# Kernel optimization log

Hardware: AMD Instinct MI355X
Metric: run time of the kernel (lower is better)

The kernel has to match this reference:

```python
import jax, jax.numpy as jnp
import numpy as np


def _fixed_bernoulli(key, heads, rows, cols, connectivity):
    # Each column gets exactly k = max(1, int(connectivity*rows)) ones (as in _fixed_bernoulli).
    k = max(1, int(connectivity * rows))
    r = jax.random.uniform(key, (heads, rows, cols))
    thr = jnp.sort(r, axis=1)[:, k - 1:k, :]  # k-th smallest per (head, col)
    return (r <= thr).astype(jnp.float32)


def _spectral_radius(W, iters=80):
    # Power-iteration estimate of |lambda_max| per head (replaces torch.linalg.eigvals at init).
    U, N, _ = W.shape
    v0 = jnp.ones((U, N), jnp.float32) / np.sqrt(N)

    def body(v, _):
        w = jnp.einsum('unm,um->un', W, v)
        nrm = jnp.linalg.norm(w, axis=-1, keepdims=True)
        return w / nrm, nrm[:, 0]

    _, nrms = jax.lax.scan(body, v0, None, length=iters)
    return jnp.mean(nrms[-10:], axis=0)  # damp oscillation from complex eigenpairs


def setup_inputs() -> dict:
    key = jax.random.key(0)
    ks = jax.random.split(key, 10)
    B, U, N, D, O = 64, 16, 2048, 1024, 1024
    X = jax.random.normal(ks[0], (B, U, D), jnp.float32)
    state = jax.random.normal(ks[1], (B, U, N), jnp.float32)
    Wmask = _fixed_bernoulli(ks[2], U, N, N, 0.2)
    W = jax.random.normal(ks[3], (U, N, N), jnp.float32) * Wmask
    W = W / _spectral_radius(W)[:, None, None]  # W buffer is normalized to spectral radius ~1
    Win = _fixed_bernoulli(ks[4], U, D, N, 0.2)  # 0/1 fixed-bernoulli input weights
    bias = (jax.random.uniform(ks[5], (U, 1, N)) < 0.5).astype(jnp.float32)
    Wout = jax.random.normal(ks[6], (U, N, O), jnp.float32)
    adaptive_lr = jax.random.uniform(ks[7], (U, D, 1), jnp.float32)
    sr = jax.random.uniform(ks[8], (U, 1, 1), jnp.float32)
    temperature = jnp.ones((1,), jnp.float32)
    return {"X": X, "state": state, "W": W, "Win": Win, "bias": bias,
            "Wout": Wout, "adaptive_lr": adaptive_lr, "sr": sr, "temperature": temperature}


def reference(X, state, W, Win, bias, Wout, adaptive_lr, sr, temperature):
    # X: [B,U,D], state: [B,U,N]
    # lr: softmax over the units axis of (X @ adaptive_lr) / temperature -> [B,U,1]
    lr = jax.nn.softmax(jnp.einsum('bud,udk->buk', X, adaptive_lr) / temperature, axis=1)
    feed = jnp.einsum('bud,udn->bun', X, Win)
    # _sparse_mm_subhead(state, W*sr, ...) + bias == per-unit state @ (W*sr) + bias
    echo = jnp.einsum('bun,unm->bum', state, W * sr) + bias[:, 0, :]
    new_state = (1.0 - lr) * state + lr * jnp.tanh(feed + echo)  # [B,U,N]
    output = jnp.einsum('bun,uno->buo', new_state, Wout)  # [B,U,O]
    return (new_state, output)
```

## Files before the change

kernel.cpp:

```cpp
#include <hip/hip_runtime.h>
#include <stdint.h>

typedef __attribute__((ext_vector_type(8))) short short8;
typedef __attribute__((ext_vector_type(4))) float f32x4;

#define BB 64
#define UU 16
#define NN 2048
#define DD 1024
#define OO 1024

static __device__ __forceinline__ float bf2f(unsigned short v){
  union { unsigned int u; float f; } c; c.u = ((unsigned int)v) << 16; return c.f;
}
static __device__ __forceinline__ unsigned short f2bf(float f){
  union { float f; unsigned int u; } c; c.f = f;
  unsigned int u = c.u;
  unsigned int r = (u + 0x7FFFu + ((u >> 16) & 1u)) >> 16;
  return (unsigned short)r;
}
static __device__ __forceinline__ bool is_bf16_buf(const void* temp){
  return ((*(const unsigned int*)temp) & 0xFFFFu) == 0x3F80u;
}
static __device__ __forceinline__ short8 cvt8(const float* p){
  f32x4 a0 = *(const f32x4*)p, a1 = *(const f32x4*)(p + 4);
  short8 r;
  #pragma unroll
  for (int j = 0; j < 4; ++j){ r[j] = (short)f2bf(a0[j]); r[4+j] = (short)f2bf(a1[j]); }
  return r;
}

union BPack { unsigned int u[4]; short8 s; };

__global__ __launch_bounds__(256)
void lr_kernel(const void* Xv, const void* alrv, const void* tempv, float* lrp)
{
  const bool isbf = is_bf16_buf(tempv);
  const int b = blockIdx.x;
  __shared__ float s[16];
  const int lane = threadIdx.x & 63;
  const int wave = threadIdx.x >> 6;
  for (int uu = 0; uu < 4; ++uu){
    const int u = wave * 4 + uu;
    float acc = 0.0f;
    if (isbf){
      const unsigned short* X = (const unsigned short*)Xv + ((size_t)(b*UU + u))*DD;
      const unsigned short* A = (const unsigned short*)alrv + (size_t)u*DD;
      for (int d = lane; d < DD; d += 64) acc += bf2f(X[d]) * bf2f(A[d]);
    } else {
      const float* X = (const float*)Xv + ((size_t)(b*UU + u))*DD;
      const float* A = (const float*)alrv + (size_t)u*DD;
      for (int d = lane; d < DD; d += 64) acc += X[d] * A[d];
    }
    #pragma unroll
    for (int off = 32; off; off >>= 1) acc += __shfl_down(acc, off, 64);
    if (lane == 0) s[u] = acc;
  }
  __syncthreads();
  if (threadIdx.x == 0){
    const float t = isbf ? bf2f(*(const unsigned short*)tempv) : *(const float*)tempv;
    float mx = -3.0e38f;
    #pragma unroll
    for (int u = 0; u < 16; ++u){ s[u] /= t; mx = fmaxf(mx, s[u]); }
    float e[16], sum = 0.0f;
    #pragma unroll
    for (int u = 0; u < 16; ++u){ e[u] = expf(s[u] - mx); sum += e[u]; }
    #pragma unroll
    for (int u = 0; u < 16; ++u) lrp[b*16 + u] = e[u] / sum;
  }
}

__global__ __launch_bounds__(256)
void ns_kernel(const void* Xv, const void* Sv, const void* Wv, const void* Winv,
               const void* biasv, const void* srv, const void* tempv,
               const float* lrp, void* outv)
{
  const bool isbf = is_bf16_buf(tempv);
  const int u    = blockIdx.y;
  const int n0   = blockIdx.x * 64;
  const int lane = threadIdx.x & 63;
  const int wave = threadIdx.x >> 6;
  const int q    = lane >> 4;
  const int m    = lane & 15;
  const int col  = n0 + wave*16 + m;

  const float srval = isbf ? bf2f(((const unsigned short*)srv)[u]) : ((const float*)srv)[u];

  int arow[4];
  #pragma unroll
  for (int mt = 0; mt < 4; ++mt) arow[mt] = (mt*16 + m)*UU + u;

  const unsigned short* Xp = (const unsigned short*)Xv;
  const unsigned short* Sp = (const unsigned short*)Sv;
  const float* Xf = (const float*)Xv;
  const float* Sf = (const float*)Sv;
  const unsigned short* Winp = (const unsigned short*)Winv + (size_t)u*DD*NN;
  const unsigned short* Wp   = (const unsigned short*)Wv   + (size_t)u*NN*NN;
  const float* Winf = (const float*)Winv + (size_t)u*DD*NN;
  const float* Wvf  = (const float*)Wv   + (size_t)u*NN*NN;

  short8 A0[4], A1[4], A2[4];
  unsigned int B0[8], B1[8], B2[8];

  auto loadA = [&](short8* A, int c){
    const int kk = c*32 + q*8;
    if (isbf){
      #pragma unroll
      for (int mt = 0; mt < 4; ++mt)
        A[mt] = (kk < DD) ? *(const short8*)(Xp + (size_t)arow[mt]*DD + kk)
                          : *(const short8*)(Sp + (size_t)arow[mt]*NN + (kk - DD));
    } else {
      #pragma unroll
      for (int mt = 0; mt < 4; ++mt)
        A[mt] = (kk < DD) ? cvt8(Xf + (size_t)arow[mt]*DD + kk)
                          : cvt8(Sf + (size_t)arow[mt]*NN + (kk - DD));
    }
  };
  auto loadB = [&](unsigned int* B, int c){
    const int kk = c*32 + q*8;
    if (isbf){
      const unsigned short* p = (kk < DD) ? Winp + (size_t)kk*NN + col
                                          : Wp   + (size_t)(kk - DD)*NN + col;
      #pragma unroll
      for (int j = 0; j < 8; ++j) B[j] = p[(size_t)j*NN];
    } else {
      const float* p = (kk < DD) ? Winf + (size_t)kk*NN + col
                                 : Wvf  + (size_t)(kk - DD)*NN + col;
      #pragma unroll
      for (int j = 0; j < 8; ++j) B[j] = f2bf(p[(size_t)j*NN]);
    }
  };

  f32x4 accF[4] = {};
  f32x4 accE[4] = {};

  auto step = [&](short8* A, unsigned int* B, bool feed){
    BPack bb;
    bb.u[0] = B[0] | (B[1] << 16);
    bb.u[1] = B[2] | (B[3] << 16);
    bb.u[2] = B[4] | (B[5] << 16);
    bb.u[3] = B[6] | (B[7] << 16);
    if (feed){
      #pragma unroll
      for (int mt = 0; mt < 4; ++mt)
        accF[mt] = __builtin_amdgcn_mfma_f32_16x16x32_bf16(A[mt], bb.s, accF[mt], 0, 0, 0);
    } else {
      #pragma unroll
      for (int mt = 0; mt < 4; ++mt)
        accE[mt] = __builtin_amdgcn_mfma_f32_16x16x32_bf16(A[mt], bb.s, accE[mt], 0, 0, 0);
    }
  };

  const int NCH = (DD + NN) / 32;
  loadA(A0, 0); loadB(B0, 0);
  loadA(A1, 1); loadB(B1, 1);
  loadA(A2, 2); loadB(B2, 2);

  #pragma unroll 1
  for (int c = 0; c < NCH; c += 3){
    step(A0, B0, c < 32);
    if (c + 3 < NCH){ loadA(A0, c + 3); loadB(B0, c + 3); }
    step(A1, B1, c + 1 < 32);
    if (c + 4 < NCH){ loadA(A1, c + 4); loadB(B1, c + 4); }
    step(A2, B2, c + 2 < 32);
    if (c + 5 < NCH){ loadA(A2, c + 5); loadB(B2, c + 5); }
  }

  {
    const float bval = isbf ? bf2f(((const unsigned short*)biasv)[u*NN + col])
                            : ((const float*)biasv)[u*NN + col];
    #pragma unroll
    for (int mt = 0; mt < 4; ++mt){
      #pragma unroll
      for (int r = 0; r < 4; ++r){
        const int b = mt*16 + q*4 + r;
        const size_t idx = ((size_t)(b*UU + u))*NN + col;
        const float l = lrp[b*UU + u];
        const float sold = isbf ? bf2f(((const unsigned short*)Sv)[idx]) : ((const float*)Sv)[idx];
        const float val = accF[mt][r] + srval*accE[mt][r] + bval;
        const float tv = tanhf(val);
        const float nsv = (1.0f - l)*sold + l*tv;
        if (isbf) ((unsigned short*)outv)[idx] = f2bf(nsv);
        else      ((float*)outv)[idx] = nsv;
      }
    }
  }
}

__global__ __launch_bounds__(256)
void out_kernel(const void* NSv, const void* Woutv, const void* tempv, void* outv)
{
  const bool isbf = is_bf16_buf(tempv);
  const int u    = blockIdx.y;
  const int n0   = blockIdx.x * 32;
  const int lane = threadIdx.x & 63;
  const int wave = threadIdx.x >> 6;
  const int wc   = wave & 1;
  const int wr   = wave >> 1;
  const int q    = lane >> 4;
  const int m    = lane & 15;
  const int col  = n0 + wc*16 + m;

  int arow[2];
  #pragma unroll
  for (int mt = 0; mt < 2; ++mt) arow[mt] = (wr*32 + mt*16 + m)*UU + u;

  const unsigned short* Ap = (const unsigned short*)NSv;
  const float* Af = (const float*)NSv;
  const unsigned short* Wo = (const unsigned short*)Woutv + (size_t)u*NN*OO;
  const float* Wof = (const float*)Woutv + (size_t)u*NN*OO;

  short8 A0[2], A1[2], A2[2];
  unsigned int B0[8], B1[8], B2[8];

  auto loadA = [&](short8* A, int c){
    const int kk = c*32 + q*8;
    if (isbf){
      #pragma unroll
      for (int mt = 0; mt < 2; ++mt)
        A[mt] = *(const short8*)(Ap + (size_t)arow[mt]*NN + kk);
    } else {
      #pragma unroll
      for (int mt = 0; mt < 2; ++mt)
        A[mt] = cvt8(Af + (size_t)arow[mt]*NN + kk);
    }
  };
  auto loadB = [&](unsigned int* B, int c){
    const int kk = c*32 + q*8;
    if (isbf){
      const unsigned short* p = Wo + (size_t)kk*OO + col;
      #pragma unroll
      for (int j = 0; j < 8; ++j) B[j] = p[(size_t)j*OO];
    } else {
      const float* p = Wof + (size_t)kk*OO + col;
      #pragma unroll
      for (int j = 0; j < 8; ++j) B[j] = f2bf(p[(size_t)j*OO]);
    }
  };

  f32x4 acc[2] = {};

  auto step = [&](short8* A, unsigned int* B){
    BPack bb;
    bb.u[0] = B[0] | (B[1] << 16);
    bb.u[1] = B[2] | (B[3] << 16);
    bb.u[2] = B[4] | (B[5] << 16);
    bb.u[3] = B[6] | (B[7] << 16);
    #pragma unroll
    for (int mt = 0; mt < 2; ++mt)
      acc[mt] = __builtin_amdgcn_mfma_f32_16x16x32_bf16(A[mt], bb.s, acc[mt], 0, 0, 0);
  };

  const int NCH = NN / 32;
  loadA(A0, 0); loadB(B0, 0);
  loadA(A1, 1); loadB(B1, 1);
  loadA(A2, 2); loadB(B2, 2);

  #pragma unroll 1
  for (int c = 0; c < NCH; c += 3){
    step(A0, B0);
    if (c + 3 < NCH){ loadA(A0, c + 3); loadB(B0, c + 3); }
    if (c + 1 < NCH){
      step(A1, B1);
      if (c + 4 < NCH){ loadA(A1, c + 4); loadB(B1, c + 4); }
    }
    if (c + 2 < NCH){
      step(A2, B2);
      if (c + 5 < NCH){ loadA(A2, c + 5); loadB(B2, c + 5); }
    }
  }

  {
    #pragma unroll
    for (int mt = 0; mt < 2; ++mt){
      #pragma unroll
      for (int r = 0; r < 4; ++r){
        const int b = wr*32 + mt*16 + q*4 + r;
        const size_t idx = ((size_t)(b*UU + u))*OO + col;
        if (isbf) ((unsigned short*)outv)[(size_t)BB*UU*NN + idx] = f2bf(acc[mt][r]);
        else      ((float*)outv)[(size_t)BB*UU*NN + idx] = acc[mt][r];
      }
    }
  }
}

extern "C" void kernel_launch(void* const* d_in, const int* in_sizes, int n_in,
                              void* d_out, int out_size, void* d_ws, size_t ws_size,
                              hipStream_t stream)
{
  const void* X    = d_in[0];
  const void* st   = d_in[1];
  const void* W    = d_in[2];
  const void* Win  = d_in[3];
  const void* bias = d_in[4];
  const void* Wout = d_in[5];
  const void* alr  = d_in[6];
  const void* sr   = d_in[7];
  const void* temp = d_in[8];

  float* lrbuf = (float*)d_ws;

  lr_kernel<<<dim3(BB), dim3(256), 0, stream>>>(X, alr, temp, lrbuf);
  ns_kernel<<<dim3(NN/64, UU), dim3(256), 0, stream>>>(X, st, W, Win, bias, sr, temp, lrbuf, d_out);
  out_kernel<<<dim3(OO/32, UU), dim3(256), 0, stream>>>(d_out, Wout, temp, d_out);
}
```

Baseline: 803.6 us.

## Stage weight tiles into LDS via global_load_lds with swizzled multi-buffer pipeline

For the bf16 path, both kernels now copy weight tiles from global memory straight into a six-deep ring of shared-memory buffers using global_load_lds. They then gather the MFMA B operands from LDS through an XOR swizzle that avoids bank conflicts. Before, each lane issued eight scalar 2-byte strided global loads per chunk. The change adds explicit vmcnt waits and a block barrier at every chunk, and the output kernel now processes 64-deep K chunks. The fp32 path is kept as before, and the hand-counted vmcnt values risk being wrong if the compiler reorders the loads.

Measured after the change: 717.7 us. 10.7% less time.

```diff
diff --git a/kernel.cpp b/kernel.cpp
--- a/kernel.cpp
+++ b/kernel.cpp
@@ -9,6 +9,9 @@
 #define NN 2048
 #define DD 1024
 #define OO 1024
+
+typedef const __attribute__((address_space(1))) unsigned int as1_u32;
+typedef __attribute__((address_space(3))) unsigned int as3_u32;
 
 static __device__ __forceinline__ float bf2f(unsigned short v){
   union { unsigned int u; float f; } c; c.u = ((unsigned int)v) << 16; return c.f;
@@ -90,80 +93,144 @@
   #pragma unroll
   for (int mt = 0; mt < 4; ++mt) arow[mt] = (mt*16 + m)*UU + u;
 
-  const unsigned short* Xp = (const unsigned short*)Xv;
-  const unsigned short* Sp = (const unsigned short*)Sv;
-  const float* Xf = (const float*)Xv;
-  const float* Sf = (const float*)Sv;
-  const unsigned short* Winp = (const unsigned short*)Winv + (size_t)u*DD*NN;
-  const unsigned short* Wp   = (const unsigned short*)Wv   + (size_t)u*NN*NN;
-  const float* Winf = (const float*)Winv + (size_t)u*DD*NN;
-  const float* Wvf  = (const float*)Wv   + (size_t)u*NN*NN;
-
-  short8 A0[4], A1[4], A2[4];
-  unsigned int B0[8], B1[8], B2[8];
-
-  auto loadA = [&](short8* A, int c){
-    const int kk = c*32 + q*8;
-    if (isbf){
-      #pragma unroll
-      for (int mt = 0; mt < 4; ++mt)
-        A[mt] = (kk < DD) ? *(const short8*)(Xp + (size_t)arow[mt]*DD + kk)
-                          : *(const short8*)(Sp + (size_t)arow[mt]*NN + (kk - DD));
-    } else {
+  f32x4 accF[4] = {};
+  f32x4 accE[4] = {};
+
+  __shared__ unsigned short Wl[6][32*64];
+
+  if (isbf){
+    const unsigned short* Xp = (const unsigned short*)Xv;
+    const unsigned short* Sp = (const unsigned short*)Sv;
+    const unsigned short* Winp = (const unsigned short*)Winv + (size_t)u*DD*NN;
+    const unsigned short* Wp   = (const unsigned short*)Wv   + (size_t)u*NN*NN;
+
+    const int G  = wave*64 + lane;
+    const int sk = G >> 3;
+    const int sg = G & 7;
+    const int skey = (sk + (sk >> 3)) & 3;
+    const int sgs  = sg ^ skey;
+
+    short8 A0[4], A1[4], A2[4];
+
+    auto loadA = [&](short8* A, int c){
+      const int kk = c*32 + q*8;
+      if (kk < DD){
+        #pragma unroll
+        for (int mt = 0; mt < 4; ++mt) A[mt] = *(const short8*)(Xp + (size_t)arow[mt]*DD + kk);
+      } else {
+        #pragma unroll
+        for (int mt = 0; mt < 4; ++mt) A[mt] = *(const short8*)(Sp + (size_t)arow[mt]*NN + (kk-DD));
+      }
+    };
+    auto stageW = [&](int c, int p){
+      const int kg = c*32 + sk;
+      const unsigned short* src = (kg < DD) ? Winp + (size_t)kg*NN + n0 + sgs*8
+                                            : Wp   + (size_t)(kg-DD)*NN + n0 + sgs*8;
+      __builtin_amdgcn_global_load_lds((as1_u32*)src, (as3_u32*)&Wl[p][wave*512], 16, 0, 0);
+    };
+    const int o2 = wave*2 + (m>>3);
+    const int ml = m & 7;
+    auto gatherB = [&](int p) -> short8 {
+      unsigned int B[8];
+      #pragma unroll
+      for (int j = 0; j < 8; ++j){
+        const int k = q*8 + j;
+        const int key = (k + (k >> 3)) & 3;
+        B[j] = Wl[p][k*64 + ((o2 ^ key) << 3) + ml];
+      }
+      BPack bb;
+      bb.u[0] = B[0] | (B[1] << 16);
+      bb.u[1] = B[2] | (B[3] << 16);
+      bb.u[2] = B[4] | (B[5] << 16);
+      bb.u[3] = B[6] | (B[7] << 16);
+      return bb.s;
+    };
+
+    stageW(0, 0); loadA(A0, 0);
+    stageW(1, 1); loadA(A1, 1);
+    stageW(2, 2);
+
+#define NS_PH(c, Acur, Anext, p) { \
+    if ((c) + 3 < 96) stageW((c)+3, ((p)+3) % 6); \
+    if ((c) + 2 < 96) loadA(Anext, (c)+2); \
+    if ((c) + 3 < 96)      { asm volatile("s_waitcnt vmcnt(11)" ::: "memory"); } \
+    else if ((c) + 2 < 96) { asm volatile("s_waitcnt vmcnt(10)" ::: "memory"); } \
+    else if ((c) + 1 < 96) { asm volatile("s_waitcnt vmcnt(5)"  ::: "memory"); } \
+    else                   { asm volatile("s_waitcnt vmcnt(0)"  ::: "memory"); } \
+    __builtin_amdgcn_s_barrier(); \
+    asm volatile("" ::: "memory"); \
+    { short8 bfv = gatherB(p); \
+      if ((c) < 32){ \
+        accF[0] = __builtin_amdgcn_mfma_f32_16x16x32_bf16(Acur[0], bfv, accF[0],0,0,0); \
+        accF[1] = __builtin_amdgcn_mfma_f32_16x16x32_bf16(Acur[1], bfv, accF[1],0,0,0); \
+        accF[2] = __builtin_amdgcn_mfma_f32_16x16x32_bf16(Acur[2], bfv, accF[2],0,0,0); \
+        accF[3] = __builtin_amdgcn_mfma_f32_16x16x32_bf16(Acur[3], bfv, accF[3],0,0,0); \
+      } else { \
+        accE[0] = __builtin_amdgcn_mfma_f32_16x16x32_bf16(Acur[0], bfv, accE[0],0,0,0); \
+        accE[1] = __builtin_amdgcn_mfma_f32_16x16x32_bf16(Acur[1], bfv, accE[1],0,0,0); \
+        accE[2] = __builtin_amdgcn_mfma_f32_16x16x32_bf16(Acur[2], bfv, accE[2],0,0,0); \
+        accE[3] = __builtin_amdgcn_mfma_f32_16x16x32_bf16(Acur[3], bfv, accE[3],0,0,0); \
+      } } }
+
+    #pragma unroll 1
+    for (int c0 = 0; c0 < 96; c0 += 6){
+      NS_PH(c0+0, A0, A2, 0);
+      NS_PH(c0+1, A1, A0, 1);
+      NS_PH(c0+2, A2, A1, 2);
+      NS_PH(c0+3, A0, A2, 3);
+      NS_PH(c0+4, A1, A0, 4);
+      NS_PH(c0+5, A2, A1, 5);
+    }
+#undef NS_PH
+  } else {
+    const float* Xf = (const float*)Xv;
+    const float* Sf = (const float*)Sv;
+    const float* Winf = (const float*)Winv + (size_t)u*DD*NN;
+    const float* Wvf  = (const float*)Wv   + (size_t)u*NN*NN;
+    short8 A0[4], A1[4], A2[4];
+    unsigned int B0[8], B1[8], B2[8];
+    auto loadA = [&](short8* A, int c){
+      const int kk = c*32 + q*8;
       #pragma unroll
       for (int mt = 0; mt < 4; ++mt)
         A[mt] = (kk < DD) ? cvt8(Xf + (size_t)arow[mt]*DD + kk)
                           : cvt8(Sf + (size_t)arow[mt]*NN + (kk - DD));
-    }
-  };
-  auto loadB = [&](unsigned int* B, int c){
-    const int kk = c*32 + q*8;
-    if (isbf){
-      const unsigned short* p = (kk < DD) ? Winp + (size_t)kk*NN + col
-                                          : Wp   + (size_t)(kk - DD)*NN + col;
-      #pragma unroll
-      for (int j = 0; j < 8; ++j) B[j] = p[(size_t)j*NN];
-    } else {
+    };
+    auto loadB = [&](unsigned int* B, int c){
+      const int kk = c*32 + q*8;
       const float* p = (kk < DD) ? Winf + (size_t)kk*NN + col
                                  : Wvf  + (size_t)(kk - DD)*NN + col;
       #pragma unroll
       for (int j = 0; j < 8; ++j) B[j] = f2bf(p[(size_t)j*NN]);
-    }
-  };
-
-  f32x4 accF[4] = {};
-  f32x4 accE[4] = {};
-
-  auto step = [&](short8* A, unsigned int* B, bool feed){
-    BPack bb;
-    bb.u[0] = B[0] | (B[1] << 16);
-    bb.u[1] = B[2] | (B[3] << 16);
-    bb.u[2] = B[4] | (B[5] << 16);
-    bb.u[3] = B[6] | (B[7] << 16);
-    if (feed){
-      #pragma unroll
-      for (int mt = 0; mt < 4; ++mt)
-        accF[mt] = __builtin_amdgcn_mfma_f32_16x16x32_bf16(A[mt], bb.s, accF[mt], 0, 0, 0);
-    } else {
-      #pragma unroll
-      for (int mt = 0; mt < 4; ++mt)
-        accE[mt] = __builtin_amdgcn_mfma_f32_16x16x32_bf16(A[mt], bb.s, accE[mt], 0, 0, 0);
-    }
-  };
-
-  const int NCH = (DD + NN) / 32;
-  loadA(A0, 0); loadB(B0, 0);
-  loadA(A1, 1); loadB(B1, 1);
-  loadA(A2, 2); loadB(B2, 2);
-
-  #pragma unroll 1
-  for (int c = 0; c < NCH; c += 3){
-    step(A0, B0, c < 32);
-    if (c + 3 < NCH){ loadA(A0, c + 3); loadB(B0, c + 3); }
-    step(A1, B1, c + 1 < 32);
-    if (c + 4 < NCH){ loadA(A1, c + 4); loadB(B1, c + 4); }
-    step(A2, B2, c + 2 < 32);
-    if (c + 5 < NCH){ loadA(A2, c + 5); loadB(B2, c + 5); }
+    };
+    auto step = [&](short8* A, unsigned int* B, bool feed){
+      BPack bb;
+      bb.u[0] = B[0] | (B[1] << 16);
+      bb.u[1] = B[2] | (B[3] << 16);
+      bb.u[2] = B[4] | (B[5] << 16);
+      bb.u[3] = B[6] | (B[7] << 16);
+      if (feed){
+        #pragma unroll
+        for (int mt = 0; mt < 4; ++mt)
+          accF[mt] = __builtin_amdgcn_mfma_f32_16x16x32_bf16(A[mt], bb.s, accF[mt], 0, 0, 0);
+      } else {
+        #pragma unroll
+        for (int mt = 0; mt < 4; ++mt)
+          accE[mt] = __builtin_amdgcn_mfma_f32_16x16x32_bf16(A[mt], bb.s, accE[mt], 0, 0, 0);
+      }
+    };
+    loadA(A0, 0); loadB(B0, 0);
+    loadA(A1, 1); loadB(B1, 1);
+    loadA(A2, 2); loadB(B2, 2);
+    #pragma unroll 1
+    for (int c = 0; c < 96; c += 3){
+      step(A0, B0, c < 32);
+      if (c + 3 < 96){ loadA(A0, c + 3); loadB(B0, c + 3); }
+      step(A1, B1, c + 1 < 32);
+      if (c + 4 < 96){ loadA(A1, c + 4); loadB(B1, c + 4); }
+      step(A2, B2, c + 2 < 32);
+      if (c + 5 < 96){ loadA(A2, c + 5); loadB(B2, c + 5); }
+    }
   }
 
   {
@@ -205,68 +272,127 @@
   #pragma unroll
   for (int mt = 0; mt < 2; ++mt) arow[mt] = (wr*32 + mt*16 + m)*UU + u;
 
-  const unsigned short* Ap = (const unsigned short*)NSv;
-  const float* Af = (const float*)NSv;
-  const unsigned short* Wo = (const unsigned short*)Woutv + (size_t)u*NN*OO;
-  const float* Wof = (const float*)Woutv + (size_t)u*NN*OO;
-
-  short8 A0[2], A1[2], A2[2];
-  unsigned int B0[8], B1[8], B2[8];
-
-  auto loadA = [&](short8* A, int c){
-    const int kk = c*32 + q*8;
-    if (isbf){
-      #pragma unroll
-      for (int mt = 0; mt < 2; ++mt)
-        A[mt] = *(const short8*)(Ap + (size_t)arow[mt]*NN + kk);
-    } else {
+  f32x4 acc[2] = {};
+
+  __shared__ unsigned short Wl[6][64*32];
+
+  if (isbf){
+    const unsigned short* Ap = (const unsigned short*)NSv;
+    const unsigned short* Wo = (const unsigned short*)Woutv + (size_t)u*NN*OO;
+
+    const int G  = wave*64 + lane;
+    const int sk = G >> 2;
+    const int sg = G & 3;
+    const int skey = (sk + (sk >> 3)) & 3;
+    const int sgs  = sg ^ skey;
+
+    short8 A0[4], A1[4], A2[4];
+
+    auto loadA = [&](short8* A, int c){
+      #pragma unroll
+      for (int kh = 0; kh < 2; ++kh){
+        const int kk = c*64 + kh*32 + q*8;
+        #pragma unroll
+        for (int mt = 0; mt < 2; ++mt)
+          A[kh*2+mt] = *(const short8*)(Ap + (size_t)arow[mt]*NN + kk);
+      }
+    };
+    auto stageW = [&](int c, int p){
+      const unsigned short* src = Wo + (size_t)(c*64 + sk)*OO + n0 + sgs*8;
+      __builtin_amdgcn_global_load_lds((as1_u32*)src, (as3_u32*)&Wl[p][wave*512], 16, 0, 0);
+    };
+    const int o2 = wc*2 + (m>>3);
+    const int ml = m & 7;
+    auto gatherB = [&](int p, int kh) -> short8 {
+      unsigned int B[8];
+      #pragma unroll
+      for (int j = 0; j < 8; ++j){
+        const int k = kh*32 + q*8 + j;
+        const int key = (k + (k >> 3)) & 3;
+        B[j] = Wl[p][k*32 + ((o2 ^ key) << 3) + ml];
+      }
+      BPack bb;
+      bb.u[0] = B[0] | (B[1] << 16);
+      bb.u[1] = B[2] | (B[3] << 16);
+      bb.u[2] = B[4] | (B[5] << 16);
+      bb.u[3] = B[6] | (B[7] << 16);
+      return bb.s;
+    };
+
+    stageW(0, 0); loadA(A0, 0);
+    stageW(1, 1); loadA(A1, 1);
+    stageW(2, 2);
+
+#define O_PH(c, Acur, Anext, p) { \
+    if ((c) + 3 < 32) stageW((c)+3, ((p)+3) % 6); \
+    if ((c) + 2 < 32) loadA(Anext, (c)+2); \
+    if ((c) + 3 < 32)      { asm volatile("s_waitcnt vmcnt(11)" ::: "memory"); } \
+    else if ((c) + 2 < 32) { asm volatile("s_waitcnt vmcnt(10)" ::: "memory"); } \
+    else if ((c) + 1 < 32) { asm volatile("s_waitcnt vmcnt(5)"  ::: "memory"); } \
+    else                   { asm volatile("s_waitcnt vmcnt(0)"  ::: "memory"); } \
+    __builtin_amdgcn_s_barrier(); \
+    asm volatile("" ::: "memory"); \
+    { short8 bf0 = gatherB(p, 0); \
+      acc[0] = __builtin_amdgcn_mfma_f32_16x16x32_bf16(Acur[0], bf0, acc[0],0,0,0); \
+      acc[1] = __builtin_amdgcn_mfma_f32_16x16x32_bf16(Acur[1], bf0, acc[1],0,0,0); \
+      short8 bf1 = gatherB(p, 1); \
+      acc[0] = __builtin_amdgcn_mfma_f32_16x16x32_bf16(Acur[2], bf1, acc[0],0,0,0); \
+      acc[1] = __builtin_amdgcn_mfma_f32_16x16x32_bf16(Acur[3], bf1, acc[1],0,0,0); } }
+
+    #pragma unroll 1
+    for (int c0 = 0; c0 < 30; c0 += 6){
+      O_PH(c0+0, A0, A2, 0);
+      O_PH(c0+1, A1, A0, 1);
+      O_PH(c0+2, A2, A1, 2);
+      O_PH(c0+3, A0, A2, 3);
+      O_PH(c0+4, A1, A0, 4);
+      O_PH(c0+5, A2, A1, 5);
+    }
+    O_PH(30, A0, A2, 0);
+    O_PH(31, A1, A0, 1);
+#undef O_PH
+  } else {
+    const float* Af = (const float*)NSv;
+    const float* Wof = (const float*)Woutv + (size_t)u*NN*OO;
+    short8 A0[2], A1[2], A2[2];
+    unsigned int B0[8], B1[8], B2[8];
+    auto loadA = [&](short8* A, int c){
+      const int kk = c*32 + q*8;
       #pragma unroll
       for (int mt = 0; mt < 2; ++mt)
         A[mt] = cvt8(Af + (size_t)arow[mt]*NN + kk);
-    }
-  };
-  auto loadB = [&](unsigned int* B, int c){
-    const int kk = c*32 + q*8;
-    if (isbf){
-      const unsigned short* p = Wo + (size_t)kk*OO + col;
-      #pragma unroll
-      for (int j = 0; j < 8; ++j) B[j] = p[(size_t)j*OO];
-    } else {
+    };
+    auto loadB = [&](unsigned int* B, int c){
+      const int kk = c*32 + q*8;
       const float* p = Wof + (size_t)kk*OO + col;
       #pragma unroll
       for (int j = 0; j < 8; ++j) B[j] = f2bf(p[(size_t)j*OO]);
-    }
-  };
-
-  f32x4 acc[2] = {};
-
-  auto step = [&](short8* A, unsigned int* B){
-    BPack bb;
-    bb.u[0] = B[0] | (B[1] << 16);
-    bb.u[1] = B[2] | (B[3] << 16);
-    bb.u[2] = B[4] | (B[5] << 16);
-    bb.u[3] = B[6] | (B[7] << 16);
-    #pragma unroll
-    for (int mt = 0; mt < 2; ++mt)
-      acc[mt] = __builtin_amdgcn_mfma_f32_16x16x32_bf16(A[mt], bb.s, acc[mt], 0, 0, 0);
-  };
-
-  const int NCH = NN / 32;
-  loadA(A0, 0); loadB(B0, 0);
-  loadA(A1, 1); loadB(B1, 1);
-  loadA(A2, 2); loadB(B2, 2);
-
-  #pragma unroll 1
-  for (int c = 0; c < NCH; c += 3){
-    step(A0, B0);
-    if (c + 3 < NCH){ loadA(A0, c + 3); loadB(B0, c + 3); }
-    if (c + 1 < NCH){
-      step(A1, B1);
-      if (c + 4 < NCH){ loadA(A1, c + 4); loadB(B1, c + 4); }
-    }
-    if (c + 2 < NCH){
-      step(A2, B2);
-      if (c + 5 < NCH){ loadA(A2, c + 5); loadB(B2, c + 5); }
+    };
+    auto step = [&](short8* A, unsigned int* B){
+      BPack bb;
+      bb.u[0] = B[0] | (B[1] << 16);
+      bb.u[1] = B[2] | (B[3] << 16);
+      bb.u[2] = B[4] | (B[5] << 16);
+      bb.u[3] = B[6] | (B[7] << 16);
+      #pragma unroll
+      for (int mt = 0; mt < 2; ++mt)
+        acc[mt] = __builtin_amdgcn_mfma_f32_16x16x32_bf16(A[mt], bb.s, acc[mt], 0, 0, 0);
+    };
+    loadA(A0, 0); loadB(B0, 0);
+    loadA(A1, 1); loadB(B1, 1);
+    loadA(A2, 2); loadB(B2, 2);
+    #pragma unroll 1
+    for (int c = 0; c < 64; c += 3){
+      step(A0, B0);
+      if (c + 3 < 64){ loadA(A0, c + 3); loadB(B0, c + 3); }
+      if (c + 1 < 64){
+        step(A1, B1);
+        if (c + 4 < 64){ loadA(A1, c + 4); loadB(B1, c + 4); }
+      }
+      if (c + 2 < 64){
+        step(A2, B2);
+        if (c + 5 < 64){ loadA(A2, c + 5); loadB(B2, c + 5); }
+      }
     }
   }
 
```

## Stage GEMM tiles through LDS with async global_load_lds multi-buffer pipeline

Applied to the files above, without the earlier changes.

Both GEMM kernels now stage activation tiles and weight tiles through shared memory. Weights are copied asynchronously with global_load_lds into a 6-deep ring buffer, and activations use a 4-deep register-to-LDS buffer, with one barrier per K-chunk. Each wave's N-tile grows to 32 columns, using even/odd interleaved B fragments unpacked from 32-bit LDS reads. Previously each lane did strided 2-byte global loads of W. The change adds heavy LDS use and per-chunk barriers, which lowers occupancy and adds sync overhead. The fp32 path becomes a simple unpipelined loop.

Result: faster. 655.3 us (-18.5%).

```diff
diff --git a/kernel.cpp b/kernel.cpp
--- a/kernel.cpp
+++ b/kernel.cpp
@@ -9,6 +9,9 @@
 #define NN 2048
 #define DD 1024
 #define OO 1024
+
+typedef const __attribute__((address_space(1))) unsigned int as1_u32;
+typedef __attribute__((address_space(3))) unsigned int as3_u32;
 
 static __device__ __forceinline__ float bf2f(unsigned short v){
   union { unsigned int u; float f; } c; c.u = ((unsigned int)v) << 16; return c.f;
@@ -77,208 +80,358 @@
 {
   const bool isbf = is_bf16_buf(tempv);
   const int u    = blockIdx.y;
-  const int n0   = blockIdx.x * 64;
-  const int lane = threadIdx.x & 63;
-  const int wave = threadIdx.x >> 6;
+  const int n0   = blockIdx.x * 128;
+  const int tid  = threadIdx.x;
+  const int lane = tid & 63;
+  const int wave = tid >> 6;
   const int q    = lane >> 4;
   const int m    = lane & 15;
-  const int col  = n0 + wave*16 + m;
 
   const float srval = isbf ? bf2f(((const unsigned short*)srv)[u]) : ((const float*)srv)[u];
 
-  int arow[4];
-  #pragma unroll
-  for (int mt = 0; mt < 4; ++mt) arow[mt] = (mt*16 + m)*UU + u;
-
-  const unsigned short* Xp = (const unsigned short*)Xv;
-  const unsigned short* Sp = (const unsigned short*)Sv;
-  const float* Xf = (const float*)Xv;
-  const float* Sf = (const float*)Sv;
-  const unsigned short* Winp = (const unsigned short*)Winv + (size_t)u*DD*NN;
-  const unsigned short* Wp   = (const unsigned short*)Wv   + (size_t)u*NN*NN;
-  const float* Winf = (const float*)Winv + (size_t)u*DD*NN;
-  const float* Wvf  = (const float*)Wv   + (size_t)u*NN*NN;
-
-  short8 A0[4], A1[4], A2[4];
-  unsigned int B0[8], B1[8], B2[8];
-
-  auto loadA = [&](short8* A, int c){
-    const int kk = c*32 + q*8;
-    if (isbf){
-      #pragma unroll
-      for (int mt = 0; mt < 4; ++mt)
-        A[mt] = (kk < DD) ? *(const short8*)(Xp + (size_t)arow[mt]*DD + kk)
-                          : *(const short8*)(Sp + (size_t)arow[mt]*NN + (kk - DD));
-    } else {
-      #pragma unroll
-      for (int mt = 0; mt < 4; ++mt)
-        A[mt] = (kk < DD) ? cvt8(Xf + (size_t)arow[mt]*DD + kk)
-                          : cvt8(Sf + (size_t)arow[mt]*NN + (kk - DD));
-    }
-  };
-  auto loadB = [&](unsigned int* B, int c){
-    const int kk = c*32 + q*8;
-    if (isbf){
-      const unsigned short* p = (kk < DD) ? Winp + (size_t)kk*NN + col
-                                          : Wp   + (size_t)(kk - DD)*NN + col;
-      #pragma unroll
-      for (int j = 0; j < 8; ++j) B[j] = p[(size_t)j*NN];
-    } else {
-      const float* p = (kk < DD) ? Winf + (size_t)kk*NN + col
-                                 : Wvf  + (size_t)(kk - DD)*NN + col;
-      #pragma unroll
-      for (int j = 0; j < 8; ++j) B[j] = f2bf(p[(size_t)j*NN]);
-    }
-  };
-
-  f32x4 accF[4] = {};
-  f32x4 accE[4] = {};
-
-  auto step = [&](short8* A, unsigned int* B, bool feed){
-    BPack bb;
-    bb.u[0] = B[0] | (B[1] << 16);
-    bb.u[1] = B[2] | (B[3] << 16);
-    bb.u[2] = B[4] | (B[5] << 16);
-    bb.u[3] = B[6] | (B[7] << 16);
-    if (feed){
-      #pragma unroll
-      for (int mt = 0; mt < 4; ++mt)
-        accF[mt] = __builtin_amdgcn_mfma_f32_16x16x32_bf16(A[mt], bb.s, accF[mt], 0, 0, 0);
-    } else {
-      #pragma unroll
-      for (int mt = 0; mt < 4; ++mt)
-        accE[mt] = __builtin_amdgcn_mfma_f32_16x16x32_bf16(A[mt], bb.s, accE[mt], 0, 0, 0);
-    }
-  };
-
-  const int NCH = (DD + NN) / 32;
-  loadA(A0, 0); loadB(B0, 0);
-  loadA(A1, 1); loadB(B1, 1);
-  loadA(A2, 2); loadB(B2, 2);
-
-  #pragma unroll 1
-  for (int c = 0; c < NCH; c += 3){
-    step(A0, B0, c < 32);
-    if (c + 3 < NCH){ loadA(A0, c + 3); loadB(B0, c + 3); }
-    step(A1, B1, c + 1 < 32);
-    if (c + 4 < NCH){ loadA(A1, c + 4); loadB(B1, c + 4); }
-    step(A2, B2, c + 2 < 32);
-    if (c + 5 < NCH){ loadA(A2, c + 5); loadB(B2, c + 5); }
+  __shared__ unsigned short As[4][64*40];
+  __shared__ unsigned short Wl[6][32*128];
+
+  f32x4 accF[4][2] = {};
+  f32x4 accE[4][2] = {};
+
+  if (isbf){
+    const unsigned short* Xp = (const unsigned short*)Xv;
+    const unsigned short* Sp = (const unsigned short*)Sv;
+    const unsigned short* Winp = (const unsigned short*)Winv + (size_t)u*DD*NN;
+    const unsigned short* Wp   = (const unsigned short*)Wv   + (size_t)u*NN*NN;
+
+    const int sr_row = tid >> 2;
+    const int sa_k   = (tid & 3) << 3;
+    const int arow40 = sr_row*40;
+    const size_t agX = (size_t)(sr_row*UU + u)*DD;
+    const size_t agS = (size_t)(sr_row*UU + u)*NN;
+    const int swk0 = wave*8 + q;
+    const int swk1 = swk0 + 4;
+    const int swn  = n0 + m*8;
+    const int wdst0 = wave*1024;
+    const int wdst1 = wave*1024 + 512;
+    const int a_rd = m*40 + q*8;
+    const int gb   = q*512 + wave*16 + m;
+
+    short8 Ag0, Ag1;
+
+#define NS_MFMA(AC, AF0, AF1, AF2, AF3, BE, BO) \
+    AC[0][0] = __builtin_amdgcn_mfma_f32_16x16x32_bf16(AF0, BE.s, AC[0][0],0,0,0); \
+    AC[0][1] = __builtin_amdgcn_mfma_f32_16x16x32_bf16(AF0, BO.s, AC[0][1],0,0,0); \
+    AC[1][0] = __builtin_amdgcn_mfma_f32_16x16x32_bf16(AF1, BE.s, AC[1][0],0,0,0); \
+    AC[1][1] = __builtin_amdgcn_mfma_f32_16x16x32_bf16(AF1, BO.s, AC[1][1],0,0,0); \
+    AC[2][0] = __builtin_amdgcn_mfma_f32_16x16x32_bf16(AF2, BE.s, AC[2][0],0,0,0); \
+    AC[2][1] = __builtin_amdgcn_mfma_f32_16x16x32_bf16(AF2, BO.s, AC[2][1],0,0,0); \
+    AC[3][0] = __builtin_amdgcn_mfma_f32_16x16x32_bf16(AF3, BE.s, AC[3][0],0,0,0); \
+    AC[3][1] = __builtin_amdgcn_mfma_f32_16x16x32_bf16(AF3, BO.s, AC[3][1],0,0,0);
+
+#define NS_PH(cc, WB, WS, AB, AW, RS) { \
+    if ((cc) + 2 < 96){ *(short8*)&As[AW][arow40 + sa_k] = (RS ? Ag1 : Ag0); } \
+    if ((cc) + 4 < 96){ \
+      const int kk = ((cc)+4)*32 + sa_k; \
+      short8 v; \
+      if (kk < DD) v = *(const short8*)(Xp + agX + kk); \
+      else         v = *(const short8*)(Sp + agS + (kk - DD)); \
+      if (RS) Ag1 = v; else Ag0 = v; \
+    } \
+    __builtin_amdgcn_sched_barrier(0); \
+    if ((cc) + 4 < 96){ \
+      const int kg = ((cc)+4)*32; \
+      if (kg < DD){ \
+        __builtin_amdgcn_global_load_lds((as1_u32*)(Winp + (size_t)(kg + swk0)*NN + swn), (as3_u32*)&Wl[WS][wdst0], 16, 0, 0); \
+        __builtin_amdgcn_global_load_lds((as1_u32*)(Winp + (size_t)(kg + swk1)*NN + swn), (as3_u32*)&Wl[WS][wdst1], 16, 0, 0); \
+      } else { \
+        __builtin_amdgcn_global_load_lds((as1_u32*)(Wp + (size_t)(kg - DD + swk0)*NN + swn), (as3_u32*)&Wl[WS][wdst0], 16, 0, 0); \
+        __builtin_amdgcn_global_load_lds((as1_u32*)(Wp + (size_t)(kg - DD + swk1)*NN + swn), (as3_u32*)&Wl[WS][wdst1], 16, 0, 0); \
+      } \
+    } \
+    if ((cc) + 2 >= 96){ asm volatile("s_waitcnt vmcnt(0)" ::: "memory"); } \
+    asm volatile("s_waitcnt lgkmcnt(0)" ::: "memory"); \
+    __builtin_amdgcn_s_barrier(); \
+    asm volatile("" ::: "memory"); \
+    { \
+      short8 af0 = *(const short8*)&As[AB][a_rd +    0]; \
+      short8 af1 = *(const short8*)&As[AB][a_rd +  640]; \
+      short8 af2 = *(const short8*)&As[AB][a_rd + 1280]; \
+      short8 af3 = *(const short8*)&As[AB][a_rd + 1920]; \
+      const unsigned int* wl32 = (const unsigned int*)&Wl[WB][0]; \
+      unsigned int rd0 = wl32[gb+0*64], rd1 = wl32[gb+1*64], rd2 = wl32[gb+2*64], rd3 = wl32[gb+3*64]; \
+      unsigned int rd4 = wl32[gb+4*64], rd5 = wl32[gb+5*64], rd6 = wl32[gb+6*64], rd7 = wl32[gb+7*64]; \
+      BPack be, bo; \
+      be.u[0] = (rd0 & 0xFFFFu) | (rd1 << 16);  bo.u[0] = (rd0 >> 16) | (rd1 & 0xFFFF0000u); \
+      be.u[1] = (rd2 & 0xFFFFu) | (rd3 << 16);  bo.u[1] = (rd2 >> 16) | (rd3 & 0xFFFF0000u); \
+      be.u[2] = (rd4 & 0xFFFFu) | (rd5 << 16);  bo.u[2] = (rd4 >> 16) | (rd5 & 0xFFFF0000u); \
+      be.u[3] = (rd6 & 0xFFFFu) | (rd7 << 16);  bo.u[3] = (rd6 >> 16) | (rd7 & 0xFFFF0000u); \
+      if ((cc) < 32){ NS_MFMA(accF, af0, af1, af2, af3, be, bo) } \
+      else          { NS_MFMA(accE, af0, af1, af2, af3, be, bo) } \
+    } }
+
+    Ag0 = *(const short8*)(Xp + agX + 0*32 + sa_k);
+    Ag1 = *(const short8*)(Xp + agX + 1*32 + sa_k);
+    __builtin_amdgcn_sched_barrier(0);
+    __builtin_amdgcn_global_load_lds((as1_u32*)(Winp + (size_t)(0*32 + swk0)*NN + swn), (as3_u32*)&Wl[0][wdst0], 16, 0, 0);
+    __builtin_amdgcn_global_load_lds((as1_u32*)(Winp + (size_t)(0*32 + swk1)*NN + swn), (as3_u32*)&Wl[0][wdst1], 16, 0, 0);
+    __builtin_amdgcn_global_load_lds((as1_u32*)(Winp + (size_t)(1*32 + swk0)*NN + swn), (as3_u32*)&Wl[1][wdst0], 16, 0, 0);
+    __builtin_amdgcn_global_load_lds((as1_u32*)(Winp + (size_t)(1*32 + swk1)*NN + swn), (as3_u32*)&Wl[1][wdst1], 16, 0, 0);
+    __builtin_amdgcn_global_load_lds((as1_u32*)(Winp + (size_t)(2*32 + swk0)*NN + swn), (as3_u32*)&Wl[2][wdst0], 16, 0, 0);
+    __builtin_amdgcn_global_load_lds((as1_u32*)(Winp + (size_t)(2*32 + swk1)*NN + swn), (as3_u32*)&Wl[2][wdst1], 16, 0, 0);
+    __builtin_amdgcn_global_load_lds((as1_u32*)(Winp + (size_t)(3*32 + swk0)*NN + swn), (as3_u32*)&Wl[3][wdst0], 16, 0, 0);
+    __builtin_amdgcn_global_load_lds((as1_u32*)(Winp + (size_t)(3*32 + swk1)*NN + swn), (as3_u32*)&Wl[3][wdst1], 16, 0, 0);
+    *(short8*)&As[0][arow40 + sa_k] = Ag0;
+    Ag0 = *(const short8*)(Xp + agX + 2*32 + sa_k);
+    *(short8*)&As[1][arow40 + sa_k] = Ag1;
+    Ag1 = *(const short8*)(Xp + agX + 3*32 + sa_k);
+    asm volatile("s_waitcnt vmcnt(8)" ::: "memory");
+    asm volatile("s_waitcnt lgkmcnt(0)" ::: "memory");
+    __builtin_amdgcn_s_barrier();
+    asm volatile("" ::: "memory");
+
+    #pragma unroll 1
+    for (int c0 = 0; c0 < 96; c0 += 12){
+      NS_PH(c0+ 0, 0, 4, 0, 2, 0)
+      NS_PH(c0+ 1, 1, 5, 1, 3, 1)
+      NS_PH(c0+ 2, 2, 0, 2, 0, 0)
+      NS_PH(c0+ 3, 3, 1, 3, 1, 1)
+      NS_PH(c0+ 4, 4, 2, 0, 2, 0)
+      NS_PH(c0+ 5, 5, 3, 1, 3, 1)
+      NS_PH(c0+ 6, 0, 4, 2, 0, 0)
+      NS_PH(c0+ 7, 1, 5, 3, 1, 1)
+      NS_PH(c0+ 8, 2, 0, 0, 2, 0)
+      NS_PH(c0+ 9, 3, 1, 1, 3, 1)
+      NS_PH(c0+10, 4, 2, 2, 0, 0)
+      NS_PH(c0+11, 5, 3, 3, 1, 1)
+    }
+#undef NS_PH
+#undef NS_MFMA
+  } else {
+    const float* Xf = (const float*)Xv;
+    const float* Sf = (const float*)Sv;
+    const float* Winf = (const float*)Winv + (size_t)u*DD*NN;
+    const float* Wvf  = (const float*)Wv   + (size_t)u*NN*NN;
+    for (int c = 0; c < 96; ++c){
+      const int kk = c*32 + q*8;
+      short8 af[4];
+      #pragma unroll
+      for (int mt = 0; mt < 4; ++mt){
+        const size_t rb = (size_t)((mt*16 + m)*UU + u);
+        af[mt] = (kk < DD) ? cvt8(Xf + rb*DD + kk) : cvt8(Sf + rb*NN + (kk - DD));
+      }
+      #pragma unroll
+      for (int g = 0; g < 2; ++g){
+        const int cl = n0 + wave*32 + g*16 + m;
+        const float* p = (kk < DD) ? Winf + (size_t)kk*NN + cl
+                                   : Wvf  + (size_t)(kk - DD)*NN + cl;
+        BPack bb;
+        unsigned int B[8];
+        #pragma unroll
+        for (int j = 0; j < 8; ++j) B[j] = f2bf(p[(size_t)j*NN]);
+        bb.u[0] = B[0] | (B[1] << 16); bb.u[1] = B[2] | (B[3] << 16);
+        bb.u[2] = B[4] | (B[5] << 16); bb.u[3] = B[6] | (B[7] << 16);
+        if (c < 32){
+          #pragma unroll
+          for (int mt = 0; mt < 4; ++mt)
+            accF[mt][g] = __builtin_amdgcn_mfma_f32_16x16x32_bf16(af[mt], bb.s, accF[mt][g],0,0,0);
+        } else {
+          #pragma unroll
+          for (int mt = 0; mt < 4; ++mt)
+            accE[mt][g] = __builtin_amdgcn_mfma_f32_16x16x32_bf16(af[mt], bb.s, accE[mt][g],0,0,0);
+        }
+      }
+    }
   }
 
   {
-    const float bval = isbf ? bf2f(((const unsigned short*)biasv)[u*NN + col])
-                            : ((const float*)biasv)[u*NN + col];
+    const int wcol = n0 + wave*32;
     #pragma unroll
     for (int mt = 0; mt < 4; ++mt){
       #pragma unroll
-      for (int r = 0; r < 4; ++r){
-        const int b = mt*16 + q*4 + r;
-        const size_t idx = ((size_t)(b*UU + u))*NN + col;
-        const float l = lrp[b*UU + u];
-        const float sold = isbf ? bf2f(((const unsigned short*)Sv)[idx]) : ((const float*)Sv)[idx];
-        const float val = accF[mt][r] + srval*accE[mt][r] + bval;
-        const float tv = tanhf(val);
-        const float nsv = (1.0f - l)*sold + l*tv;
-        if (isbf) ((unsigned short*)outv)[idx] = f2bf(nsv);
-        else      ((float*)outv)[idx] = nsv;
+      for (int eo = 0; eo < 2; ++eo){
+        const int cl = isbf ? (wcol + 2*m + eo) : (wcol + eo*16 + m);
+        const float bval = isbf ? bf2f(((const unsigned short*)biasv)[u*NN + cl])
+                                : ((const float*)biasv)[u*NN + cl];
+        #pragma unroll
+        for (int r = 0; r < 4; ++r){
+          const int b = mt*16 + q*4 + r;
+          const size_t idx = ((size_t)(b*UU + u))*NN + cl;
+          const float l = lrp[b*UU + u];
+          const float sold = isbf ? bf2f(((const unsigned short*)Sv)[idx]) : ((const float*)Sv)[idx];
+          const float val = accF[mt][eo][r] + srval*accE[mt][eo][r] + bval;
+          const float tv = tanhf(val);
+          const float nsv = (1.0f - l)*sold + l*tv;
+          if (isbf) ((unsigned short*)outv)[idx] = f2bf(nsv);
+          else      ((float*)outv)[idx] = nsv;
+        }
       }
     }
   }
 }
 
-__global__ __launch_bounds__(256)
+__global__ __launch_bounds__(128)
 void out_kernel(const void* NSv, const void* Woutv, const void* tempv, void* outv)
 {
   const bool isbf = is_bf16_buf(tempv);
   const int u    = blockIdx.y;
-  const int n0   = blockIdx.x * 32;
-  const int lane = threadIdx.x & 63;
-  const int wave = threadIdx.x >> 6;
-  const int wc   = wave & 1;
-  const int wr   = wave >> 1;
+  const int n0   = blockIdx.x * 64;
+  const int tid  = threadIdx.x;
+  const int lane = tid & 63;
+  const int wave = tid >> 6;
   const int q    = lane >> 4;
   const int m    = lane & 15;
-  const int col  = n0 + wc*16 + m;
-
-  int arow[2];
-  #pragma unroll
-  for (int mt = 0; mt < 2; ++mt) arow[mt] = (wr*32 + mt*16 + m)*UU + u;
-
-  const unsigned short* Ap = (const unsigned short*)NSv;
-  const float* Af = (const float*)NSv;
-  const unsigned short* Wo = (const unsigned short*)Woutv + (size_t)u*NN*OO;
-  const float* Wof = (const float*)Woutv + (size_t)u*NN*OO;
-
-  short8 A0[2], A1[2], A2[2];
-  unsigned int B0[8], B1[8], B2[8];
-
-  auto loadA = [&](short8* A, int c){
-    const int kk = c*32 + q*8;
-    if (isbf){
-      #pragma unroll
-      for (int mt = 0; mt < 2; ++mt)
-        A[mt] = *(const short8*)(Ap + (size_t)arow[mt]*NN + kk);
-    } else {
-      #pragma unroll
-      for (int mt = 0; mt < 2; ++mt)
-        A[mt] = cvt8(Af + (size_t)arow[mt]*NN + kk);
-    }
-  };
-  auto loadB = [&](unsigned int* B, int c){
-    const int kk = c*32 + q*8;
-    if (isbf){
-      const unsigned short* p = Wo + (size_t)kk*OO + col;
-      #pragma unroll
-      for (int j = 0; j < 8; ++j) B[j] = p[(size_t)j*OO];
-    } else {
-      const float* p = Wof + (size_t)kk*OO + col;
-      #pragma unroll
-      for (int j = 0; j < 8; ++j) B[j] = f2bf(p[(size_t)j*OO]);
-    }
-  };
-
-  f32x4 acc[2] = {};
-
-  auto step = [&](short8* A, unsigned int* B){
-    BPack bb;
-    bb.u[0] = B[0] | (B[1] << 16);
-    bb.u[1] = B[2] | (B[3] << 16);
-    bb.u[2] = B[4] | (B[5] << 16);
-    bb.u[3] = B[6] | (B[7] << 16);
-    #pragma unroll
-    for (int mt = 0; mt < 2; ++mt)
-      acc[mt] = __builtin_amdgcn_mfma_f32_16x16x32_bf16(A[mt], bb.s, acc[mt], 0, 0, 0);
-  };
-
-  const int NCH = NN / 32;
-  loadA(A0, 0); loadB(B0, 0);
-  loadA(A1, 1); loadB(B1, 1);
-  loadA(A2, 2); loadB(B2, 2);
-
-  #pragma unroll 1
-  for (int c = 0; c < NCH; c += 3){
-    step(A0, B0);
-    if (c + 3 < NCH){ loadA(A0, c + 3); loadB(B0, c + 3); }
-    if (c + 1 < NCH){
-      step(A1, B1);
-      if (c + 4 < NCH){ loadA(A1, c + 4); loadB(B1, c + 4); }
-    }
-    if (c + 2 < NCH){
-      step(A2, B2);
-      if (c + 5 < NCH){ loadA(A2, c + 5); loadB(B2, c + 5); }
+
+  __shared__ unsigned short As2[4][64*40];
+  __shared__ unsigned short Wl2[6][32*64];
+
+  f32x4 acc[4][2] = {};
+
+  if (isbf){
+    const unsigned short* NSp = (const unsigned short*)NSv;
+    const unsigned short* Wo  = (const unsigned short*)Woutv + (size_t)u*NN*OO;
+
+    const int sr_row = tid >> 1;
+    const int sa_k   = (tid & 1) << 4;
+    const int arow40 = sr_row*40;
+    const size_t agN = (size_t)(sr_row*UU + u)*NN;
+    const int swk0 = wave*16 + (lane >> 3);
+    const int swk1 = swk0 + 8;
+    const int swn  = n0 + (lane & 7)*8;
+    const int wdst0 = wave*1024;
+    const int wdst1 = wave*1024 + 512;
+    const int a_rd = m*40 + q*8;
+    const int gb   = q*256 + wave*16 + m;
+
+    short8 Ag0a, Ag0b, Ag1a, Ag1b;
+
+#define O_PH(cc, WB, WS, AB, AW, RS) { \
+    if ((cc) + 2 < 64){ \
+      *(short8*)&As2[AW][arow40 + sa_k]     = (RS ? Ag1a : Ag0a); \
+      *(short8*)&As2[AW][arow40 + sa_k + 8] = (RS ? Ag1b : Ag0b); \
+    } \
+    if ((cc) + 4 < 64){ \
+      const int kk = ((cc)+4)*32 + sa_k; \
+      short8 va = *(const short8*)(NSp + agN + kk); \
+      short8 vb = *(const short8*)(NSp + agN + kk + 8); \
+      if (RS){ Ag1a = va; Ag1b = vb; } else { Ag0a = va; Ag0b = vb; } \
+    } \
+    __builtin_amdgcn_sched_barrier(0); \
+    if ((cc) + 4 < 64){ \
+      const int kg = ((cc)+4)*32; \
+      __builtin_amdgcn_global_load_lds((as1_u32*)(Wo + (size_t)(kg + swk0)*OO + swn), (as3_u32*)&Wl2[WS][wdst0], 16, 0, 0); \
+      __builtin_amdgcn_global_load_lds((as1_u32*)(Wo + (size_t)(kg + swk1)*OO + swn), (as3_u32*)&Wl2[WS][wdst1], 16, 0, 0); \
+    } \
+    if ((cc) + 2 >= 64){ asm volatile("s_waitcnt vmcnt(0)" ::: "memory"); } \
+    asm volatile("s_waitcnt lgkmcnt(0)" ::: "memory"); \
+    __builtin_amdgcn_s_barrier(); \
+    asm volatile("" ::: "memory"); \
+    { \
+      short8 af0 = *(const short8*)&As2[AB][a_rd +    0]; \
+      short8 af1 = *(const short8*)&As2[AB][a_rd +  640]; \
+      short8 af2 = *(const short8*)&As2[AB][a_rd + 1280]; \
+      short8 af3 = *(const short8*)&As2[AB][a_rd + 1920]; \
+      const unsigned int* wl32 = (const unsigned int*)&Wl2[WB][0]; \
+      unsigned int rd0 = wl32[gb+0*32], rd1 = wl32[gb+1*32], rd2 = wl32[gb+2*32], rd3 = wl32[gb+3*32]; \
+      unsigned int rd4 = wl32[gb+4*32], rd5 = wl32[gb+5*32], rd6 = wl32[gb+6*32], rd7 = wl32[gb+7*32]; \
+      BPack be, bo; \
+      be.u[0] = (rd0 & 0xFFFFu) | (rd1 << 16);  bo.u[0] = (rd0 >> 16) | (rd1 & 0xFFFF0000u); \
+      be.u[1] = (rd2 & 0xFFFFu) | (rd3 << 16);  bo.u[1] = (rd2 >> 16) | (rd3 & 0xFFFF0000u); \
+      be.u[2] = (rd4 & 0xFFFFu) | (rd5 << 16);  bo.u[2] = (rd4 >> 16) | (rd5 & 0xFFFF0000u); \
+      be.u[3] = (rd6 & 0xFFFFu) | (rd7 << 16);  bo.u[3] = (rd6 >> 16) | (rd7 & 0xFFFF0000u); \
+      acc[0][0] = __builtin_amdgcn_mfma_f32_16x16x32_bf16(af0, be.s, acc[0][0],0,0,0); \
+      acc[0][1] = __builtin_amdgcn_mfma_f32_16x16x32_bf16(af0, bo.s, acc[0][1],0,0,0); \
+      acc[1][0] = __builtin_amdgcn_mfma_f32_16x16x32_bf16(af1, be.s, acc[1][0],0,0,0); \
+      acc[1][1] = __builtin_amdgcn_mfma_f32_16x16x32_bf16(af1, bo.s, acc[1][1],0,0,0); \
+      acc[2][0] = __builtin_amdgcn_mfma_f32_16x16x32_bf16(af2, be.s, acc[2][0],0,0,0); \
+      acc[2][1] = __builtin_amdgcn_mfma_f32_16x16x32_bf16(af2, bo.s, acc[2][1],0,0,0); \
+      acc[3][0] = __builtin_amdgcn_mfma_f32_16x16x32_bf16(af3, be.s, acc[3][0],0,0,0); \
+      acc[3][1] = __builtin_amdgcn_mfma_f32_16x16x32_bf16(af3, bo.s, acc[3][1],0,0,0); \
+    } }
+
+    Ag0a = *(const short8*)(NSp + agN + 0*32 + sa_k);
+    Ag0b = *(const short8*)(NSp + agN + 0*32 + sa_k + 8);
+    Ag1a = *(const short8*)(NSp + agN + 1*32 + sa_k);
+    Ag1b = *(const short8*)(NSp + agN + 1*32 + sa_k + 8);
+    __builtin_amdgcn_sched_barrier(0);
+    __builtin_amdgcn_global_load_lds((as1_u32*)(Wo + (size_t)(0*32 + swk0)*OO + swn), (as3_u32*)&Wl2[0][wdst0], 16, 0, 0);
+    __builtin_amdgcn_global_load_lds((as1_u32*)(Wo + (size_t)(0*32 + swk1)*OO + swn), (as3_u32*)&Wl2[0][wdst1], 16, 0, 0);
+    __builtin_amdgcn_global_load_lds((as1_u32*)(Wo + (size_t)(1*32 + swk0)*OO + swn), (as3_u32*)&Wl2[1][wdst0], 16, 0, 0);
+    __builtin_amdgcn_global_load_lds((as1_u32*)(Wo + (size_t)(1*32 + swk1)*OO + swn), (as3_u32*)&Wl2[1][wdst1], 16, 0, 0);
+    __builtin_amdgcn_global_load_lds((as1_u32*)(Wo + (size_t)(2*32 + swk0)*OO + swn), (as3_u32*)&Wl2[2][wdst0], 16, 0, 0);
+    __builtin_amdgcn_global_load_lds((as1_u32*)(Wo + (size_t)(2*32 + swk1)*OO + swn), (as3_u32*)&Wl2[2][wdst1], 16, 0, 0);
+    __builtin_amdgcn_global_load_lds((as1_u32*)(Wo + (size_t)(3*32 + swk0)*OO + swn), (as3_u32*)&Wl2[3][wdst0], 16, 0, 0);
+    __builtin_amdgcn_global_load_lds((as1_u32*)(Wo + (size_t)(3*32 + swk1)*OO + swn), (as3_u32*)&Wl2[3][wdst1], 16, 0, 0);
+    *(short8*)&As2[0][arow40 + sa_k]     = Ag0a;
+    *(short8*)&As2[0][arow40 + sa_k + 8] = Ag0b;
+    Ag0a = *(const short8*)(NSp + agN + 2*32 + sa_k);
+    Ag0b = *(const short8*)(NSp + agN + 2*32 + sa_k + 8);
+    *(short8*)&As2[1][arow40 + sa_k]     = Ag1a;
+    *(short8*)&As2[1][arow40 + sa_k + 8] = Ag1b;
+    Ag1a = *(const short8*)(NSp + agN + 3*32 + sa_k);
+    Ag1b = *(const short8*)(NSp + agN + 3*32 + sa_k + 8);
+    asm volatile("s_waitcnt vmcnt(10)" ::: "memory");
+    asm volatile("s_waitcnt lgkmcnt(0)" ::: "memory");
+    __builtin_amdgcn_s_barrier();
+    asm volatile("" ::: "memory");
+
+    #pragma unroll 1
+    for (int c0 = 0; c0 < 60; c0 += 12){
+      O_PH(c0+ 0, 0, 4, 0, 2, 0)
+      O_PH(c0+ 1, 1, 5, 1, 3, 1)
+      O_PH(c0+ 2, 2, 0, 2, 0, 0)
+      O_PH(c0+ 3, 3, 1, 3, 1, 1)
+      O_PH(c0+ 4, 4, 2, 0, 2, 0)
+      O_PH(c0+ 5, 5, 3, 1, 3, 1)
+      O_PH(c0+ 6, 0, 4, 2, 0, 0)
+      O_PH(c0+ 7, 1, 5, 3, 1, 1)
+      O_PH(c0+ 8, 2, 0, 0, 2, 0)
+      O_PH(c0+ 9, 3, 1, 1, 3, 1)
+      O_PH(c0+10, 4, 2, 2, 0, 0)
+      O_PH(c0+11, 5, 3, 3, 1, 1)
+    }
+    O_PH(60, 0, 4, 0, 2, 0)
+    O_PH(61, 1, 5, 1, 3, 1)
+    O_PH(62, 2, 0, 2, 0, 0)
+    O_PH(63, 3, 1, 3, 1, 1)
+#undef O_PH
+  } else {
+    const float* Af  = (const float*)NSv;
+    const float* Wof = (const float*)Woutv + (size_t)u*NN*OO;
+    for (int c = 0; c < 64; ++c){
+      const int kk = c*32 + q*8;
+      short8 af[4];
+      #pragma unroll
+      for (int mt = 0; mt < 4; ++mt)
+        af[mt] = cvt8(Af + (size_t)((mt*16 + m)*UU + u)*NN + kk);
+      #pragma unroll
+      for (int g = 0; g < 2; ++g){
+        const int cl = n0 + wave*32 + g*16 + m;
+        const float* p = Wof + (size_t)kk*OO + cl;
+        BPack bb;
+        unsigned int B[8];
+        #pragma unroll
+        for (int j = 0; j < 8; ++j) B[j] = f2bf(p[(size_t)j*OO]);
+        bb.u[0] = B[0] | (B[1] << 16); bb.u[1] = B[2] | (B[3] << 16);
+        bb.u[2] = B[4] | (B[5] << 16); bb.u[3] = B[6] | (B[7] << 16);
+        #pragma unroll
+        for (int mt = 0; mt < 4; ++mt)
+          acc[mt][g] = __builtin_amdgcn_mfma_f32_16x16x32_bf16(af[mt], bb.s, acc[mt][g],0,0,0);
+      }
     }
   }
 
   {
-    #pragma unroll
-    for (int mt = 0; mt < 2; ++mt){
-      #pragma unroll
-      for (int r = 0; r < 4; ++r){
-        const int b = wr*32 + mt*16 + q*4 + r;
-        const size_t idx = ((size_t)(b*UU + u))*OO + col;
-        if (isbf) ((unsigned short*)outv)[(size_t)BB*UU*NN + idx] = f2bf(acc[mt][r]);
-        else      ((float*)outv)[(size_t)BB*UU*NN + idx] = acc[mt][r];
+    const int wcol = n0 + wave*32;
+    #pragma unroll
+    for (int mt = 0; mt < 4; ++mt){
+      #pragma unroll
+      for (int eo = 0; eo < 2; ++eo){
+        const int cl = isbf ? (wcol + 2*m + eo) : (wcol + eo*16 + m);
+        #pragma unroll
+        for (int r = 0; r < 4; ++r){
+          const int b = mt*16 + q*4 + r;
+          const size_t idx = ((size_t)(b*UU + u))*OO + cl;
+          if (isbf) ((unsigned short*)outv)[(size_t)BB*UU*NN + idx] = f2bf(acc[mt][eo][r]);
+          else      ((float*)outv)[(size_t)BB*UU*NN + idx] = acc[mt][eo][r];
+        }
       }
     }
   }
@@ -301,6 +454,6 @@
   float* lrbuf = (float*)d_ws;
 
   lr_kernel<<<dim3(BB), dim3(256), 0, stream>>>(X, alr, temp, lrbuf);
-  ns_kernel<<<dim3(NN/64, UU), dim3(256), 0, stream>>>(X, st, W, Win, bias, sr, temp, lrbuf, d_out);
-  out_kernel<<<dim3(OO/32, UU), dim3(256), 0, stream>>>(d_out, Wout, temp, d_out);
-}
+  ns_kernel<<<dim3(NN/128, UU), dim3(256), 0, stream>>>(X, st, W, Win, bias, sr, temp, lrbuf, d_out);
+  out_kernel<<<dim3(OO/64, UU), dim3(128), 0, stream>>>(d_out, Wout, temp, d_out);
+}
```
